# Kernel tuning notes

Measured on AMD Instinct MI355X. Metric: run time of the kernel, lower is better.

Reference implementation:

```python
import jax, jax.numpy as jnp
import numpy as np

B, NPG = 128, 512            # graphs, nodes per graph (batch is contiguous & uniform)
N = B * NPG                  # 65536 nodes
DEG = 8
E = N * DEG                  # 524288 edges
F_IN, NHID = 128, 64
H, C = 3, NHID               # GAT heads, out channels per head
HC = H * C                   # 192
NCLS = 10
RATIO = 0.5
NEG_SLOPE = 0.2


def setup_inputs() -> dict:
    key = jax.random.key(0)
    ks = jax.random.split(key, 24)
    x = jax.random.normal(ks[0], (N, F_IN), jnp.float32)
    # edges constrained within each graph (graphs are contiguous blocks of NPG nodes)
    offs = jnp.repeat(jnp.arange(B, dtype=jnp.int32) * NPG, NPG * DEG)
    src = jax.random.randint(ks[1], (E,), 0, NPG, dtype=jnp.int32) + offs
    dst = jax.random.randint(ks[2], (E,), 0, NPG, dtype=jnp.int32) + offs
    edge_index = jnp.stack([src, dst], axis=0)
    edge_attr = jax.random.normal(ks[3], (E, 2), jnp.float32)
    batch = jnp.repeat(jnp.arange(B, dtype=jnp.int32), NPG)

    def lin(k, o, i):
        return jax.random.normal(k, (o, i), jnp.float32) / np.float32(np.sqrt(i))

    return {
        "x": x, "edge_index": edge_index, "edge_attr": edge_attr, "batch": batch,
        # lin: num_features -> nhid//2
        "W_lin": lin(ks[4], NHID // 2, F_IN), "b_lin": jnp.zeros((NHID // 2,), jnp.float32),
        # GATConv(nhid//2 -> nhid, heads=3, edge_dim=2)
        "W_src": lin(ks[5], HC, NHID // 2),
        "att_src": jax.random.normal(ks[6], (H, C), jnp.float32) / np.float32(np.sqrt(C)),
        "att_dst": jax.random.normal(ks[7], (H, C), jnp.float32) / np.float32(np.sqrt(C)),
        "W_edge": lin(ks[8], HC, 2),
        "att_edge": jax.random.normal(ks[9], (H, C), jnp.float32) / np.float32(np.sqrt(C)),
        "b_gat": jnp.zeros((HC,), jnp.float32),
        # SAGPool score layer: GCNConv(nhid*3 -> 1)
        "W_gcn": lin(ks[10], 1, HC), "b_gcn": jnp.zeros((1,), jnp.float32),
        # classifier MLP
        "W1": lin(ks[11], NHID, 2 * HC), "b1": jnp.zeros((NHID,), jnp.float32),
        "W2": lin(ks[12], NHID // 2, NHID), "b2": jnp.zeros((NHID // 2,), jnp.float32),
        "W3": lin(ks[13], NCLS, NHID // 2), "b3": jnp.zeros((NCLS,), jnp.float32),
    }


def reference(x, edge_index, edge_attr, batch,
              W_lin, b_lin, W_src, att_src, att_dst, W_edge, att_edge, b_gat,
              W_gcn, b_gcn, W1, b1, W2, b2, W3, b3):
    src, dst = edge_index[0], edge_index[1]

    # ---- lin + ELU -------------------------------------------------------
    h = jax.nn.elu(x @ W_lin.T + b_lin)                       # [N, nhid//2]

    # ---- GATConv(heads=3, edge_dim=2), add_self_loops fill_value='mean' --
    loop = jnp.arange(N, dtype=src.dtype)
    cnt = jax.ops.segment_sum(jnp.ones((E,), h.dtype), dst, num_segments=N)
    loop_attr = jax.ops.segment_sum(edge_attr, dst, num_segments=N) / jnp.maximum(cnt, 1.0)[:, None]
    s_full = jnp.concatenate([src, loop])
    d_full = jnp.concatenate([dst, loop])
    ea_full = jnp.concatenate([edge_attr, loop_attr], axis=0)  # [E+N, 2]

    xp = (h @ W_src.T).reshape(N, H, C)                        # projected per-head feats
    a_src = (xp * att_src).sum(-1)                             # [N, H]
    a_dst = (xp * att_dst).sum(-1)                             # [N, H]
    ef = (ea_full @ W_edge.T).reshape(-1, H, C)
    a_edge = (ef * att_edge).sum(-1)                           # [E+N, H]

    alpha = jax.nn.leaky_relu(a_src[s_full] + a_dst[d_full] + a_edge, NEG_SLOPE)
    m = jax.ops.segment_max(alpha, d_full, num_segments=N)     # scatter-softmax over dst
    ealpha = jnp.exp(alpha - m[d_full])
    denom = jax.ops.segment_sum(ealpha, d_full, num_segments=N)
    alpha = ealpha / (denom[d_full] + 1e-16)                   # [E+N, H]

    out = jax.ops.segment_sum(alpha[:, :, None] * xp[s_full], d_full, num_segments=N)
    x1 = jax.nn.relu(out.reshape(N, HC) + b_gat)               # [N, 192]

    # ---- SAGPool: GCNConv score + per-graph top-k (mask form) ------------
    xw = x1 @ W_gcn.T                                          # [N, 1]
    deg = jax.ops.segment_sum(jnp.ones((E,), x1.dtype), dst, num_segments=N) + 1.0
    dinv = jax.lax.rsqrt(deg)
    agg = jax.ops.segment_sum((dinv[src] * dinv[dst])[:, None] * xw[src], dst, num_segments=N)
    score = (agg + (dinv ** 2)[:, None] * xw + b_gcn)[:, 0]    # [N]

    k = int(np.ceil(RATIO * NPG))                              # nodes kept per graph
    s2 = score.reshape(B, NPG)
    rank = jnp.argsort(jnp.argsort(-s2, axis=1), axis=1)
    mask = rank < k                                            # [B, NPG] top-k selection

    xs = (x1 * jnp.tanh(score)[:, None]).reshape(B, NPG, HC)
    gmp = jnp.max(jnp.where(mask[:, :, None], xs, -jnp.inf), axis=1)   # [B, 192]
    gap = jnp.sum(jnp.where(mask[:, :, None], xs, 0.0), axis=1) / k    # [B, 192]
    r = jnp.concatenate([gmp, gap], axis=1)                    # [B, 384]

    # ---- classifier MLP (dropout is identity in eval) ---------------------
    r = jax.nn.relu(r @ W1.T + b1)
    r = jax.nn.relu(r @ W2.T + b2)
    return jax.nn.log_softmax(r @ W3.T + b3, axis=-1)          # [B, num_classes]
```

## Files before the change

### kernel.cpp

```cpp
#include <hip/hip_runtime.h>
#include <hip/hip_bf16.h>
#include <math.h>

#define NN   65536
#define EE   524288
#define BB   128
#define NPGC 512
#define HCC  192
#define KSEL 256
#define NEG  0.2f
#define PSEG 8
#define SEGN (NPGC / PSEG)
#define MAXD 40
#define SLOTS ((size_t)NN * MAXD)
#define EPG   4096

__global__ __launch_bounds__(256) void k_prep(
    const float* __restrict__ W_lin, const float* __restrict__ W_src,
    const float* __restrict__ W_edge, const float* __restrict__ att_edge,
    float* __restrict__ WlT, float* __restrict__ WsT,
    float* __restrict__ acoef, float* __restrict__ zregf) {
    int gid = blockIdx.x * 256 + threadIdx.x;
    for (int i = gid; i < NN * 6; i += NN) zregf[(size_t)NN * 3 + i] = 0.f;
    if (gid < 4096) {
        int j = gid >> 7, k = gid & 127;
        WlT[k * 32 + j] = W_lin[gid];
    }
    if (gid < 6144) {
        int j = gid >> 5, k = gid & 31;
        WsT[k * 192 + j] = W_src[gid];
    }
    if (blockIdx.x == 8) {
        __shared__ float red[6];
        int t = threadIdx.x;
        if (t < 6) red[t] = 0.f;
        __syncthreads();
        if (t < 192) {
            float ae = att_edge[t];
            int h = t >> 6;
            atomicAdd(&red[h],     W_edge[2 * t]     * ae);
            atomicAdd(&red[3 + h], W_edge[2 * t + 1] * ae);
        }
        __syncthreads();
        if (t < 6) acoef[t] = red[t];
    }
}

__device__ __forceinline__ int nodeblock_base(int bx) {
    int xcd = bx & 7, j = bx >> 3;
    int g = xcd + 8 * (j >> 1);
    return g * NPGC + (j & 1) * 256;
}

__global__ __launch_bounds__(256) void k_h(
    const float* __restrict__ x, const float* __restrict__ WlT,
    const float* __restrict__ b_lin, float* __restrict__ hbuf) {
    __shared__ float Wl[128 * 16];
    int t = threadIdx.x;
    int half = blockIdx.y;
#pragma unroll
    for (int i = 0; i < 8; ++i) {
        int idx = t + i * 256;
        int k = idx >> 4, jj = idx & 15;
        Wl[idx] = WlT[k * 32 + half * 16 + jj];
    }
    __syncthreads();
    int n = nodeblock_base(blockIdx.x) + t;
    const float4* xr = (const float4*)(x + (size_t)n * 128);
    float acc[16];
#pragma unroll
    for (int j = 0; j < 16; ++j) acc[j] = b_lin[half * 16 + j];
#pragma unroll 4
    for (int q = 0; q < 32; ++q) {
        float4 a = xr[q];
        const float* w = &Wl[(q * 4) * 16];
#pragma unroll
        for (int j = 0; j < 16; ++j) {
            acc[j] += a.x * w[j] + a.y * w[16 + j] +
                      a.z * w[32 + j] + a.w * w[48 + j];
        }
    }
#pragma unroll
    for (int j = 0; j < 16; ++j)
        acc[j] = acc[j] > 0.f ? acc[j] : expm1f(acc[j]);
    float4* dst = (float4*)(hbuf + (size_t)n * 32 + half * 16);
#pragma unroll
    for (int q = 0; q < 4; ++q)
        dst[q] = make_float4(acc[4 * q], acc[4 * q + 1],
                             acc[4 * q + 2], acc[4 * q + 3]);
}

__global__ __launch_bounds__(256) void k_xp(
    const float* __restrict__ hbuf, const float* __restrict__ WsT,
    const float* __restrict__ att_src, const float* __restrict__ att_dst,
    float* __restrict__ xp, float* __restrict__ a_src, float* __restrict__ a_dst) {
    int n = nodeblock_base(blockIdx.x) + threadIdx.x;
    int h = blockIdx.y;
    int ch = blockIdx.z;
    const float4* hr = (const float4*)(hbuf + (size_t)n * 32);
    float acc[32];
#pragma unroll
    for (int c = 0; c < 32; ++c) acc[c] = 0.f;
#pragma unroll
    for (int q = 0; q < 8; ++q) {
        float4 hv = hr[q];
        const float* w = WsT + (q * 4) * 192 + h * 64 + ch * 32;
#pragma unroll
        for (int c = 0; c < 32; ++c) {
            acc[c] += hv.x * w[c] + hv.y * w[192 + c] +
                      hv.z * w[384 + c] + hv.w * w[576 + c];
        }
    }
    float as = 0.f, ad = 0.f;
    const float* ats = att_src + h * 64 + ch * 32;
    const float* atd = att_dst + h * 64 + ch * 32;
#pragma unroll
    for (int c = 0; c < 32; ++c) {
        as += acc[c] * ats[c];
        ad += acc[c] * atd[c];
    }
    atomicAdd(&a_src[n * 3 + h], as);
    atomicAdd(&a_dst[n * 3 + h], ad);
    float4* dst = (float4*)(xp + (size_t)n * HCC + h * 64 + ch * 32);
#pragma unroll
    for (int q = 0; q < 8; ++q)
        dst[q] = make_float4(acc[4 * q], acc[4 * q + 1],
                             acc[4 * q + 2], acc[4 * q + 3]);
}

__global__ __launch_bounds__(512) void k_edges(
    const int* __restrict__ ei, const float* __restrict__ ea,
    const float* __restrict__ a_src, const float* __restrict__ a_dst,
    const float* __restrict__ acoef,
    int* __restrict__ fill, float* __restrict__ la,
    float4* __restrict__ slotA) {
    __shared__ int   s_cnt[NPGC], s_pos[NPGC];
    __shared__ float s_la[NPGC * 2];
    __shared__ float s_as[NPGC * 3], s_ad[NPGC * 3];
    int b = blockIdx.x, t = threadIdx.x;
    int g = (b & 7) + 8 * (b >> 3);
    int nbase = g * NPGC;
    int ebase = g * EPG;
    s_cnt[t] = 0; s_pos[t] = 0;
    s_la[t] = 0.f; s_la[NPGC + t] = 0.f;
    for (int i = t; i < NPGC * 3; i += 512) {
        s_as[i] = a_src[(size_t)nbase * 3 + i];
        s_ad[i] = a_dst[(size_t)nbase * 3 + i];
    }
    __syncthreads();
#pragma unroll
    for (int k = 0; k < 8; ++k) {
        int e = ebase + t + k * 512;
        int dl = ei[EE + e] & (NPGC - 1);
        atomicAdd(&s_cnt[dl], 1);
        atomicAdd(&s_la[2 * dl],     ea[2 * e]);
        atomicAdd(&s_la[2 * dl + 1], ea[2 * e + 1]);
    }
    __syncthreads();
    fill[nbase + t] = s_cnt[t];
    ((float2*)la)[nbase + t] = make_float2(s_la[2 * t], s_la[2 * t + 1]);
    float ac[6];
#pragma unroll
    for (int h = 0; h < 6; ++h) ac[h] = acoef[h];
#pragma unroll
    for (int k = 0; k < 8; ++k) {
        int e = ebase + t + k * 512;
        int s = ei[e], d = ei[EE + e];
        int sl = s & (NPGC - 1), dl = d & (NPGC - 1);
        float e0 = ea[2 * e], e1 = ea[2 * e + 1];
        float v[3];
#pragma unroll
        for (int h = 0; h < 3; ++h) {
            float a = s_as[sl * 3 + h] + s_ad[dl * 3 + h] +
                      e0 * ac[h] + e1 * ac[3 + h];
            v[h] = a >= 0.f ? a : NEG * a;
        }
        int pos = atomicAdd(&s_pos[dl], 1);
        if (pos < MAXD - 1)
            slotA[(size_t)d * MAXD + 1 + pos] =
                make_float4(v[0], v[1], v[2], __int_as_float(s));
    }
}

__global__ __launch_bounds__(256) void k_agg(
    const int* __restrict__ fill, const float4* __restrict__ slotA,
    const float* __restrict__ la,
    const float* __restrict__ a_src, const float* __restrict__ a_dst,
    const float* __restrict__ acoef, const float* __restrict__ xp,
    const float* __restrict__ b_gat, const float* __restrict__ W_gcn,
    float* __restrict__ x1, float* __restrict__ xw, float* __restrict__ dinv) {
    __shared__ float4 wsl[4][64];
    int wave = threadIdx.x >> 6, lane = threadIdx.x & 63;
    int b = blockIdx.x;
    int xcd = b & 7, j = b >> 3;
    int g = (j >> 7) * 8 + xcd;
    int n = g * NPGC + (j & 127) * 4 + wave;

    int ctrue = fill[n];
    int cnt = ctrue < (MAXD - 1) ? ctrue : (MAXD - 1);
    int tot = cnt + 1;

    float4 ent;
    if (lane == 0) {
        float inv = 1.f / fmaxf((float)ctrue, 1.f);
        float l0 = la[2 * n] * inv, l1 = la[2 * n + 1] * inv;
        float e[3];
#pragma unroll
        for (int h = 0; h < 3; ++h) {
            float v = a_src[n * 3 + h] + a_dst[n * 3 + h] +
                      l0 * acoef[h] + l1 * acoef[3 + h];
            v = v >= 0.f ? v : NEG * v;
            e[h] = __expf(v);
        }
        ent = make_float4(e[0], e[1], e[2], __int_as_float(n));
    } else if (lane <= cnt) {
        float4 pk = slotA[(size_t)n * MAXD + lane];
        ent = make_float4(__expf(pk.x), __expf(pk.y), __expf(pk.z), pk.w);
    } else {
        ent = make_float4(0.f, 0.f, 0.f, 0.f);
    }
    wsl[wave][lane] = ent;

    int head = lane >> 4;
    bool act = lane < 48;
    const float4* xp4 = (const float4*)xp;
    float ax = 0.f, ay = 0.f, az = 0.f, aw = 0.f, den = 0.f;
    int s = 0;
    for (; s + 1 < tot; s += 2) {
        float4 eA = wsl[wave][s];
        float4 eB = wsl[wave][s + 1];
        float wA = head == 0 ? eA.x : (head == 1 ? eA.y : eA.z);
        float wB = head == 0 ? eB.x : (head == 1 ? eB.y : eB.z);
        den += wA + wB;
        if (act) {
            int srcA = __float_as_int(eA.w);
            int srcB = __float_as_int(eB.w);
            float4 vA = xp4[(size_t)srcA * 48 + lane];
            float4 vB = xp4[(size_t)srcB * 48 + lane];
            ax += wA * vA.x + wB * vB.x;
            ay += wA * vA.y + wB * vB.y;
            az += wA * vA.z + wB * vB.z;
            aw += wA * vA.w + wB * vB.w;
        }
    }
    if (s < tot) {
        float4 eA = wsl[wave][s];
        float wA = head == 0 ? eA.x : (head == 1 ? eA.y : eA.z);
        den += wA;
        if (act) {
            int srcA = __float_as_int(eA.w);
            float4 vA = xp4[(size_t)srcA * 48 + lane];
            ax += wA * vA.x; ay += wA * vA.y; az += wA * vA.z; aw += wA * vA.w;
        }
    }
    float p = 0.f;
    if (act) {
        float id = 1.f / (den + 1e-16f);
        float4 bg = ((const float4*)b_gat)[lane];
        float4 v;
        v.x = fmaxf(ax * id + bg.x, 0.f);
        v.y = fmaxf(ay * id + bg.y, 0.f);
        v.z = fmaxf(az * id + bg.z, 0.f);
        v.w = fmaxf(aw * id + bg.w, 0.f);
        ((float4*)x1)[(size_t)n * 48 + lane] = v;
        float4 wg = ((const float4*)W_gcn)[lane];
        p = v.x * wg.x + v.y * wg.y + v.z * wg.z + v.w * wg.w;
    }
#pragma unroll
    for (int msk = 32; msk > 0; msk >>= 1) p += __shfl_xor(p, msk, 64);
    if (lane == 0) {
        xw[n] = p;
        dinv[n] = rsqrtf((float)ctrue + 1.f);
    }
}

__global__ void k_score(const int* __restrict__ fill, const float4* __restrict__ slotA,
                        const float* __restrict__ xw, const float* __restrict__ dinv,
                        const float* __restrict__ b_gcn, float* __restrict__ score) {
    int n = nodeblock_base(blockIdx.x) + threadIdx.x;
    int ctrue = fill[n];
    int cnt = ctrue < (MAXD - 1) ? ctrue : (MAXD - 1);
    float acc = dinv[n] * xw[n];
    const float* sA = (const float*)slotA;
    size_t base = (size_t)n * MAXD;
    for (int s = 1; s <= cnt; ++s) {
        int src = __float_as_int(sA[(base + s) * 4 + 3]);
        acc += dinv[src] * xw[src];
    }
    score[n] = b_gcn[0] + dinv[n] * acc;
}

__global__ __launch_bounds__(192) void k_poolrank(
    const float* __restrict__ score, const float* __restrict__ x1,
    float* __restrict__ pmax, float* __restrict__ psum) {
    __shared__ float sc[NPGC];
    __shared__ float ts_s[SEGN];
    __shared__ int sel_s[SEGN];
    int b = blockIdx.x;
    int xcd = b & 7, gslot = (b >> 3) & 15, seg = b >> 7;
    int g = gslot * 8 + xcd;
    int t = threadIdx.x;
    int gbase = g * NPGC;
    for (int i = t; i < NPGC; i += 192) sc[i] = score[gbase + i];
    __syncthreads();
    if (t < SEGN) {
        int iloc = seg * SEGN + t;
        float si = sc[iloc];
        int rank = 0;
        for (int j = 0; j < NPGC; ++j) {
            float sj = sc[j];
            rank += (sj > si) || (sj == si && j < iloc);
        }
        sel_s[t] = (rank < KSEL) ? 1 : 0;
        ts_s[t] = tanhf(si);
    }
    __syncthreads();
    int nb = gbase + seg * SEGN;
    float mx = -1e30f, sm = 0.f;
    for (int i = 0; i < SEGN; ++i) {
        if (sel_s[i]) {
            float v = x1[(size_t)(nb + i) * HCC + t] * ts_s[i];
            mx = fmaxf(mx, v);
            sm += v;
        }
    }
    size_t pb = (size_t)(g * PSEG + seg) * HCC + t;
    pmax[pb] = mx;
    psum[pb] = sm;
}

__global__ __launch_bounds__(384) void k_mlp(
    const float* __restrict__ pmax, const float* __restrict__ psum,
    const float* __restrict__ W1, const float* __restrict__ b1,
    const float* __restrict__ W2, const float* __restrict__ b2,
    const float* __restrict__ W3, const float* __restrict__ b3,
    float* __restrict__ out) {
    __shared__ float rs[384], part[384], h1[64], h2[32], lg[10], mls;
    int g = blockIdx.x, t = threadIdx.x;
    if (t < HCC) {
        float mx = -1e30f, sm = 0.f;
#pragma unroll
        for (int s = 0; s < PSEG; ++s) {
            mx = fmaxf(mx, pmax[(size_t)(g * PSEG + s) * HCC + t]);
            sm += psum[(size_t)(g * PSEG + s) * HCC + t];
        }
        rs[t] = mx;
        rs[HCC + t] = sm * (1.f / (float)KSEL);
    }
    __syncthreads();
    {
        int o = t / 6, sl = t - o * 6;
        const float* wr = W1 + o * 384 + sl * 64;
        const float* rr = rs + sl * 64;
        float s = 0.f;
#pragma unroll 8
        for (int k = 0; k < 64; ++k) s += rr[k] * wr[k];
        part[t] = s;
    }
    __syncthreads();
    if (t < 64) {
        float s = b1[t];
#pragma unroll
        for (int j = 0; j < 6; ++j) s += part[t * 6 + j];
        h1[t] = fmaxf(s, 0.f);
    }
    __syncthreads();
    if (t < 256) {
        int o = t >> 3, sl = t & 7;
        const float* wr = W2 + o * 64 + sl * 8;
        const float* hr = h1 + sl * 8;
        float s = 0.f;
#pragma unroll
        for (int k = 0; k < 8; ++k) s += hr[k] * wr[k];
        part[t] = s;
    }
    __syncthreads();
    if (t < 32) {
        float s = b2[t];
#pragma unroll
        for (int j = 0; j < 8; ++j) s += part[t * 8 + j];
        h2[t] = fmaxf(s, 0.f);
    }
    __syncthreads();
    if (t < 10) {
        float s = b3[t];
        for (int k = 0; k < 32; ++k) s += h2[k] * W3[t * 32 + k];
        lg[t] = s;
    }
    __syncthreads();
    if (t == 0) {
        float mx = lg[0];
        for (int j = 1; j < 10; ++j) mx = fmaxf(mx, lg[j]);
        float se = 0.f;
        for (int j = 0; j < 10; ++j) se += expf(lg[j] - mx);
        mls = mx + logf(se);
    }
    __syncthreads();
    if (t < 10) out[g * 10 + t] = lg[t] - mls;
}

extern "C" void kernel_launch(void* const* d_in, const int* in_sizes, int n_in,
                              void* d_out, int out_size, void* d_ws, size_t ws_size,
                              hipStream_t stream) {
    const float* x        = (const float*)d_in[0];
    const int*   ei       = (const int*)d_in[1];
    const float* ea       = (const float*)d_in[2];
    const float* W_lin    = (const float*)d_in[4];
    const float* b_lin    = (const float*)d_in[5];
    const float* W_src    = (const float*)d_in[6];
    const float* att_src  = (const float*)d_in[7];
    const float* att_dst  = (const float*)d_in[8];
    const float* W_edge   = (const float*)d_in[9];
    const float* att_edge = (const float*)d_in[10];
    const float* b_gat    = (const float*)d_in[11];
    const float* W_gcn    = (const float*)d_in[12];
    const float* b_gcn    = (const float*)d_in[13];
    const float* W1 = (const float*)d_in[14]; const float* b1 = (const float*)d_in[15];
    const float* W2 = (const float*)d_in[16]; const float* b2 = (const float*)d_in[17];
    const float* W3 = (const float*)d_in[18]; const float* b3 = (const float*)d_in[19];
    float* out = (float*)d_out;

    char* ws = (char*)d_ws;
    size_t off = 0;
    auto alloc = [&](size_t bytes) {
        size_t r = off;
        off += (bytes + 255) & ~(size_t)255;
        return r;
    };
    float* xp      = (float*)(ws + alloc((size_t)NN * HCC * 4));
    float* x1      = (float*)(ws + alloc((size_t)NN * HCC * 4));
    float* hbuf    = (float*)(ws + alloc((size_t)NN * 32 * 4));
    float* zregf   = (float*)(ws + alloc((size_t)NN * 9 * 4));
    int*   fill    = (int*)zregf;
    float* la      = zregf + NN;
    float* a_src   = zregf + 3 * NN;
    float* a_dst   = zregf + 6 * NN;
    float4* slotA  = (float4*)(ws + alloc(SLOTS * 16));
    float* xw      = (float*)(ws + alloc((size_t)NN * 4));
    float* dinv    = (float*)(ws + alloc((size_t)NN * 4));
    float* score   = (float*)(ws + alloc((size_t)NN * 4));
    float* acoef   = (float*)(ws + alloc(8 * 4));
    float* WlT     = (float*)(ws + alloc(4096 * 4));
    float* WsT     = (float*)(ws + alloc(6144 * 4));
    float* pmax    = (float*)(ws + alloc((size_t)BB * PSEG * HCC * 4));
    float* psum    = (float*)(ws + alloc((size_t)BB * PSEG * HCC * 4));

    k_prep<<<256, 256, 0, stream>>>(W_lin, W_src, W_edge, att_edge,
                                    WlT, WsT, acoef, zregf);
    k_h<<<dim3(256, 2), 256, 0, stream>>>(x, WlT, b_lin, hbuf);
    k_xp<<<dim3(256, 3, 2), 256, 0, stream>>>(hbuf, WsT, att_src, att_dst,
                                              xp, a_src, a_dst);
    k_edges<<<BB, 512, 0, stream>>>(ei, ea, a_src, a_dst, acoef,
                                    fill, la, slotA);
    k_agg<<<NN / 4, 256, 0, stream>>>(fill, slotA, la, a_src, a_dst,
                                      acoef, xp, b_gat, W_gcn, x1, xw, dinv);
    k_score<<<NN / 256, 256, 0, stream>>>(fill, slotA, xw, dinv, b_gcn, score);
    k_poolrank<<<BB * PSEG, 192, 0, stream>>>(score, x1, pmax, psum);
    k_mlp<<<BB, 384, 0, stream>>>(pmax, psum, W1, b1, W2, b2, W3, b3, out);
}
```

Baseline: 264.2 us.

## Drop atomics and zeroing, widen edge kernel, wave-per-node score, unroll aggregation

k_xp no longer atomically accumulates attention partials into a zeroed buffer. It writes the two channel-half partials separately, and the consumers sum them, so k_prep no longer zeroes a large region and launches far fewer blocks. k_edges runs with 1024 threads per graph. k_agg gathers four neighbours per iteration and pre-multiplies xw by dinv. k_score becomes wave-per-node with a shuffle reduction instead of a serial per-thread loop. Together these aim to cut memset traffic, atomics and gather latency, at the cost of extra partial-buffer storage and more blocks for the score step.

```diff
diff --git a/kernel.cpp b/kernel.cpp
--- a/kernel.cpp
+++ b/kernel.cpp
@@ -19,9 +19,8 @@
     const float* __restrict__ W_lin, const float* __restrict__ W_src,
     const float* __restrict__ W_edge, const float* __restrict__ att_edge,
     float* __restrict__ WlT, float* __restrict__ WsT,
-    float* __restrict__ acoef, float* __restrict__ zregf) {
+    float* __restrict__ acoef) {
     int gid = blockIdx.x * 256 + threadIdx.x;
-    for (int i = gid; i < NN * 6; i += NN) zregf[(size_t)NN * 3 + i] = 0.f;
     if (gid < 4096) {
         int j = gid >> 7, k = gid & 127;
         WlT[k * 32 + j] = W_lin[gid];
@@ -30,7 +29,7 @@
         int j = gid >> 5, k = gid & 31;
         WsT[k * 192 + j] = W_src[gid];
     }
-    if (blockIdx.x == 8) {
+    if (blockIdx.x == 24) {
         __shared__ float red[6];
         int t = threadIdx.x;
         if (t < 6) red[t] = 0.f;
@@ -93,7 +92,7 @@
 __global__ __launch_bounds__(256) void k_xp(
     const float* __restrict__ hbuf, const float* __restrict__ WsT,
     const float* __restrict__ att_src, const float* __restrict__ att_dst,
-    float* __restrict__ xp, float* __restrict__ a_src, float* __restrict__ a_dst) {
+    float* __restrict__ xp, float* __restrict__ ap_s, float* __restrict__ ap_d) {
     int n = nodeblock_base(blockIdx.x) + threadIdx.x;
     int h = blockIdx.y;
     int ch = blockIdx.z;
@@ -119,8 +118,8 @@
         as += acc[c] * ats[c];
         ad += acc[c] * atd[c];
     }
-    atomicAdd(&a_src[n * 3 + h], as);
-    atomicAdd(&a_dst[n * 3 + h], ad);
+    ap_s[((size_t)n * 3 + h) * 2 + ch] = as;
+    ap_d[((size_t)n * 3 + h) * 2 + ch] = ad;
     float4* dst = (float4*)(xp + (size_t)n * HCC + h * 64 + ch * 32);
 #pragma unroll
     for (int q = 0; q < 8; ++q)
@@ -128,9 +127,9 @@
                              acc[4 * q + 2], acc[4 * q + 3]);
 }
 
-__global__ __launch_bounds__(512) void k_edges(
+__global__ __launch_bounds__(1024) void k_edges(
     const int* __restrict__ ei, const float* __restrict__ ea,
-    const float* __restrict__ a_src, const float* __restrict__ a_dst,
+    const float* __restrict__ ap_s, const float* __restrict__ ap_d,
     const float* __restrict__ acoef,
     int* __restrict__ fill, float* __restrict__ la,
     float4* __restrict__ slotA) {
@@ -141,30 +140,36 @@
     int g = (b & 7) + 8 * (b >> 3);
     int nbase = g * NPGC;
     int ebase = g * EPG;
-    s_cnt[t] = 0; s_pos[t] = 0;
-    s_la[t] = 0.f; s_la[NPGC + t] = 0.f;
-    for (int i = t; i < NPGC * 3; i += 512) {
-        s_as[i] = a_src[(size_t)nbase * 3 + i];
-        s_ad[i] = a_dst[(size_t)nbase * 3 + i];
-    }
-    __syncthreads();
-#pragma unroll
-    for (int k = 0; k < 8; ++k) {
-        int e = ebase + t + k * 512;
+    if (t < NPGC) { s_cnt[t] = 0; s_pos[t] = 0; }
+    s_la[t] = 0.f;
+    const float2* aps2 = (const float2*)ap_s;
+    const float2* apd2 = (const float2*)ap_d;
+    for (int i = t; i < NPGC * 3; i += 1024) {
+        float2 ps = aps2[(size_t)nbase * 3 + i];
+        float2 pd = apd2[(size_t)nbase * 3 + i];
+        s_as[i] = ps.x + ps.y;
+        s_ad[i] = pd.x + pd.y;
+    }
+    __syncthreads();
+#pragma unroll
+    for (int k = 0; k < 4; ++k) {
+        int e = ebase + t + k * 1024;
         int dl = ei[EE + e] & (NPGC - 1);
         atomicAdd(&s_cnt[dl], 1);
         atomicAdd(&s_la[2 * dl],     ea[2 * e]);
         atomicAdd(&s_la[2 * dl + 1], ea[2 * e + 1]);
     }
     __syncthreads();
-    fill[nbase + t] = s_cnt[t];
-    ((float2*)la)[nbase + t] = make_float2(s_la[2 * t], s_la[2 * t + 1]);
+    if (t < NPGC) {
+        fill[nbase + t] = s_cnt[t];
+        ((float2*)la)[nbase + t] = make_float2(s_la[2 * t], s_la[2 * t + 1]);
+    }
     float ac[6];
 #pragma unroll
     for (int h = 0; h < 6; ++h) ac[h] = acoef[h];
 #pragma unroll
-    for (int k = 0; k < 8; ++k) {
-        int e = ebase + t + k * 512;
+    for (int k = 0; k < 4; ++k) {
+        int e = ebase + t + k * 1024;
         int s = ei[e], d = ei[EE + e];
         int sl = s & (NPGC - 1), dl = d & (NPGC - 1);
         float e0 = ea[2 * e], e1 = ea[2 * e + 1];
@@ -185,10 +190,10 @@
 __global__ __launch_bounds__(256) void k_agg(
     const int* __restrict__ fill, const float4* __restrict__ slotA,
     const float* __restrict__ la,
-    const float* __restrict__ a_src, const float* __restrict__ a_dst,
+    const float* __restrict__ ap_s, const float* __restrict__ ap_d,
     const float* __restrict__ acoef, const float* __restrict__ xp,
     const float* __restrict__ b_gat, const float* __restrict__ W_gcn,
-    float* __restrict__ x1, float* __restrict__ xw, float* __restrict__ dinv) {
+    float* __restrict__ x1, float* __restrict__ xwd, float* __restrict__ dinv) {
     __shared__ float4 wsl[4][64];
     int wave = threadIdx.x >> 6, lane = threadIdx.x & 63;
     int b = blockIdx.x;
@@ -204,10 +209,14 @@
     if (lane == 0) {
         float inv = 1.f / fmaxf((float)ctrue, 1.f);
         float l0 = la[2 * n] * inv, l1 = la[2 * n + 1] * inv;
+        const float2* aps2 = (const float2*)ap_s;
+        const float2* apd2 = (const float2*)ap_d;
         float e[3];
 #pragma unroll
         for (int h = 0; h < 3; ++h) {
-            float v = a_src[n * 3 + h] + a_dst[n * 3 + h] +
+            float2 ps = aps2[(size_t)n * 3 + h];
+            float2 pd = apd2[(size_t)n * 3 + h];
+            float v = (ps.x + ps.y) + (pd.x + pd.y) +
                       l0 * acoef[h] + l1 * acoef[3 + h];
             v = v >= 0.f ? v : NEG * v;
             e[h] = __expf(v);
@@ -226,30 +235,31 @@
     const float4* xp4 = (const float4*)xp;
     float ax = 0.f, ay = 0.f, az = 0.f, aw = 0.f, den = 0.f;
     int s = 0;
-    for (; s + 1 < tot; s += 2) {
-        float4 eA = wsl[wave][s];
-        float4 eB = wsl[wave][s + 1];
+    for (; s + 3 < tot; s += 4) {
+        float4 eA = wsl[wave][s],     eB = wsl[wave][s + 1];
+        float4 eC = wsl[wave][s + 2], eD = wsl[wave][s + 3];
         float wA = head == 0 ? eA.x : (head == 1 ? eA.y : eA.z);
         float wB = head == 0 ? eB.x : (head == 1 ? eB.y : eB.z);
-        den += wA + wB;
+        float wC = head == 0 ? eC.x : (head == 1 ? eC.y : eC.z);
+        float wD = head == 0 ? eD.x : (head == 1 ? eD.y : eD.z);
+        den += (wA + wB) + (wC + wD);
         if (act) {
-            int srcA = __float_as_int(eA.w);
-            int srcB = __float_as_int(eB.w);
-            float4 vA = xp4[(size_t)srcA * 48 + lane];
-            float4 vB = xp4[(size_t)srcB * 48 + lane];
-            ax += wA * vA.x + wB * vB.x;
-            ay += wA * vA.y + wB * vB.y;
-            az += wA * vA.z + wB * vB.z;
-            aw += wA * vA.w + wB * vB.w;
-        }
-    }
-    if (s < tot) {
+            float4 vA = xp4[(size_t)__float_as_int(eA.w) * 48 + lane];
+            float4 vB = xp4[(size_t)__float_as_int(eB.w) * 48 + lane];
+            float4 vC = xp4[(size_t)__float_as_int(eC.w) * 48 + lane];
+            float4 vD = xp4[(size_t)__float_as_int(eD.w) * 48 + lane];
+            ax += wA * vA.x + wB * vB.x + wC * vC.x + wD * vD.x;
+            ay += wA * vA.y + wB * vB.y + wC * vC.y + wD * vD.y;
+            az += wA * vA.z + wB * vB.z + wC * vC.z + wD * vD.z;
+            aw += wA * vA.w + wB * vB.w + wC * vC.w + wD * vD.w;
+        }
+    }
+    for (; s < tot; ++s) {
         float4 eA = wsl[wave][s];
         float wA = head == 0 ? eA.x : (head == 1 ? eA.y : eA.z);
         den += wA;
         if (act) {
-            int srcA = __float_as_int(eA.w);
-            float4 vA = xp4[(size_t)srcA * 48 + lane];
+            float4 vA = xp4[(size_t)__float_as_int(eA.w) * 48 + lane];
             ax += wA * vA.x; ay += wA * vA.y; az += wA * vA.z; aw += wA * vA.w;
         }
     }
@@ -269,25 +279,35 @@
 #pragma unroll
     for (int msk = 32; msk > 0; msk >>= 1) p += __shfl_xor(p, msk, 64);
     if (lane == 0) {
-        xw[n] = p;
-        dinv[n] = rsqrtf((float)ctrue + 1.f);
-    }
-}
-
-__global__ void k_score(const int* __restrict__ fill, const float4* __restrict__ slotA,
-                        const float* __restrict__ xw, const float* __restrict__ dinv,
-                        const float* __restrict__ b_gcn, float* __restrict__ score) {
-    int n = nodeblock_base(blockIdx.x) + threadIdx.x;
+        float dv = rsqrtf((float)ctrue + 1.f);
+        xwd[n] = p * dv;
+        dinv[n] = dv;
+    }
+}
+
+__global__ __launch_bounds__(256) void k_score(
+    const int* __restrict__ fill, const float4* __restrict__ slotA,
+    const float* __restrict__ xwd, const float* __restrict__ dinv,
+    const float* __restrict__ b_gcn, float* __restrict__ score) {
+    int wave = threadIdx.x >> 6, lane = threadIdx.x & 63;
+    int b = blockIdx.x;
+    int xcd = b & 7, j = b >> 3;
+    int g = (j >> 7) * 8 + xcd;
+    int n = g * NPGC + (j & 127) * 4 + wave;
+
     int ctrue = fill[n];
     int cnt = ctrue < (MAXD - 1) ? ctrue : (MAXD - 1);
-    float acc = dinv[n] * xw[n];
-    const float* sA = (const float*)slotA;
-    size_t base = (size_t)n * MAXD;
-    for (int s = 1; s <= cnt; ++s) {
-        int src = __float_as_int(sA[(base + s) * 4 + 3]);
-        acc += dinv[src] * xw[src];
-    }
-    score[n] = b_gcn[0] + dinv[n] * acc;
+    float acc = 0.f;
+    if (lane == 0) {
+        acc = xwd[n];
+    } else if (lane <= cnt) {
+        int src = __float_as_int(
+            ((const float*)slotA)[((size_t)n * MAXD + lane) * 4 + 3]);
+        acc = xwd[src];
+    }
+#pragma unroll
+    for (int msk = 32; msk > 0; msk >>= 1) acc += __shfl_xor(acc, msk, 64);
+    if (lane == 0) score[n] = b_gcn[0] + dinv[n] * acc;
 }
 
 __global__ __launch_bounds__(192) void k_poolrank(
@@ -430,13 +450,12 @@
     float* xp      = (float*)(ws + alloc((size_t)NN * HCC * 4));
     float* x1      = (float*)(ws + alloc((size_t)NN * HCC * 4));
     float* hbuf    = (float*)(ws + alloc((size_t)NN * 32 * 4));
-    float* zregf   = (float*)(ws + alloc((size_t)NN * 9 * 4));
-    int*   fill    = (int*)zregf;
-    float* la      = zregf + NN;
-    float* a_src   = zregf + 3 * NN;
-    float* a_dst   = zregf + 6 * NN;
+    int*   fill    = (int*)(ws + alloc((size_t)NN * 4));
+    float* la      = (float*)(ws + alloc((size_t)NN * 2 * 4));
+    float* ap_s    = (float*)(ws + alloc((size_t)NN * 6 * 4));
+    float* ap_d    = (float*)(ws + alloc((size_t)NN * 6 * 4));
     float4* slotA  = (float4*)(ws + alloc(SLOTS * 16));
-    float* xw      = (float*)(ws + alloc((size_t)NN * 4));
+    float* xwd     = (float*)(ws + alloc((size_t)NN * 4));
     float* dinv    = (float*)(ws + alloc((size_t)NN * 4));
     float* score   = (float*)(ws + alloc((size_t)NN * 4));
     float* acoef   = (float*)(ws + alloc(8 * 4));
@@ -445,16 +464,16 @@
     float* pmax    = (float*)(ws + alloc((size_t)BB * PSEG * HCC * 4));
     float* psum    = (float*)(ws + alloc((size_t)BB * PSEG * HCC * 4));
 
-    k_prep<<<256, 256, 0, stream>>>(W_lin, W_src, W_edge, att_edge,
-                                    WlT, WsT, acoef, zregf);
+    k_prep<<<25, 256, 0, stream>>>(W_lin, W_src, W_edge, att_edge,
+                                   WlT, WsT, acoef);
     k_h<<<dim3(256, 2), 256, 0, stream>>>(x, WlT, b_lin, hbuf);
     k_xp<<<dim3(256, 3, 2), 256, 0, stream>>>(hbuf, WsT, att_src, att_dst,
-                                              xp, a_src, a_dst);
-    k_edges<<<BB, 512, 0, stream>>>(ei, ea, a_src, a_dst, acoef,
-                                    fill, la, slotA);
-    k_agg<<<NN / 4, 256, 0, stream>>>(fill, slotA, la, a_src, a_dst,
-                                      acoef, xp, b_gat, W_gcn, x1, xw, dinv);
-    k_score<<<NN / 256, 256, 0, stream>>>(fill, slotA, xw, dinv, b_gcn, score);
+                                              xp, ap_s, ap_d);
+    k_edges<<<BB, 1024, 0, stream>>>(ei, ea, ap_s, ap_d, acoef,
+                                     fill, la, slotA);
+    k_agg<<<NN / 4, 256, 0, stream>>>(fill, slotA, la, ap_s, ap_d,
+                                      acoef, xp, b_gat, W_gcn, x1, xwd, dinv);
+    k_score<<<NN / 4, 256, 0, stream>>>(fill, slotA, xwd, dinv, b_gcn, score);
     k_poolrank<<<BB * PSEG, 192, 0, stream>>>(score, x1, pmax, psum);
     k_mlp<<<BB, 384, 0, stream>>>(pmax, psum, W1, b1, W2, b2, W3, b3, out);
 }
```

Measured after the change: 276.3 us. 4.6% more time.
